# Kernel tuning notes

Hardware: AMD Instinct MI355X
Metric: run time of the kernel (lower is better)

The kernel has to match this reference:

```python
import math
import jax, jax.numpy as jnp
import numpy as np

H = 16
D_MODEL = 1024
D_K = D_MODEL // H


def setup_inputs() -> dict:
    key = jax.random.key(0)
    ks = jax.random.split(key, 12)
    B, S = 4, 2048
    scale = 1.0 / math.sqrt(D_MODEL)
    inp = {
        "query": jax.random.normal(ks[0], (B, S, D_MODEL), jnp.float32),
        "key": jax.random.normal(ks[1], (B, S, D_MODEL), jnp.float32),
        "value": jax.random.normal(ks[2], (B, S, D_MODEL), jnp.float32),
        "mask": jnp.ones((B, 1, 1, S), jnp.int32),
        "Wq": jax.random.normal(ks[3], (D_MODEL, D_MODEL), jnp.float32) * scale,
        "bq": jnp.zeros((D_MODEL,), jnp.float32),
        "Wk": jax.random.normal(ks[4], (D_MODEL, D_MODEL), jnp.float32) * scale,
        "bk": jnp.zeros((D_MODEL,), jnp.float32),
        "Wv": jax.random.normal(ks[5], (D_MODEL, D_MODEL), jnp.float32) * scale,
        "bv": jnp.zeros((D_MODEL,), jnp.float32),
        "Wo": jax.random.normal(ks[6], (D_MODEL, D_MODEL), jnp.float32) * scale,
        "bo": jnp.zeros((D_MODEL,), jnp.float32),
    }
    return inp


def _split_heads(x, W, b):
    # x: (B, S, d_model) -> (B, H, S, d_k); torch Linear: x @ W.T + b
    B, S, _ = x.shape
    y = x @ W.T + b
    return y.reshape(B, S, H, D_K).transpose(0, 2, 1, 3)


def reference(query, key, value, mask, Wq, bq, Wk, bk, Wv, bv, Wo, bo):
    B, Sq, _ = query.shape
    q = _split_heads(query, Wq, bq)   # (B,H,Sq,dk)
    k = _split_heads(key, Wk, bk)     # (B,H,Skv,dk)
    v = _split_heads(value, Wv, bv)   # (B,H,Skv,dk)
    scores = jnp.einsum('bhqd,bhkd->bhqk', q, k) / math.sqrt(D_K)
    scores = jnp.where(mask == 0, jnp.float32(-1e9), scores)
    p_attn = jax.nn.softmax(scores, axis=-1)  # dropout p=0 (eval)
    x = jnp.einsum('bhqk,bhkd->bhqd', p_attn, v)
    x = x.transpose(0, 2, 1, 3).reshape(B, Sq, H * D_K)
    return x @ Wo.T + bo
```

## Files before the change

### kernel.cpp

```cpp
#include <hip/hip_runtime.h>
#include <hip/hip_bf16.h>
#include <stdint.h>

typedef unsigned short u16;
typedef short bf16x8 __attribute__((ext_vector_type(8)));
typedef float f32x4 __attribute__((ext_vector_type(4)));

#define D_MODEL 1024
#define NHEAD 16
#define DK 64
#define SEQ 2048
#define NB 4
#define MTOT (NB * SEQ)

__device__ __forceinline__ u16 f2bf(float f) {
  union { float f; unsigned u; } x; x.f = f;
  unsigned r = x.u + 0x7FFFu + ((x.u >> 16) & 1u);
  return (u16)(r >> 16);
}
#if __has_builtin(__builtin_amdgcn_cvt_pk_bf16_f32)
__device__ __forceinline__ unsigned pkbf(float a, float b) {
  auto r = __builtin_amdgcn_cvt_pk_bf16_f32(a, b);
  union { decltype(r) v; unsigned u; } c; c.v = r; return c.u;
}
#else
__device__ __forceinline__ unsigned pkbf(float a, float b) {
  return (unsigned)f2bf(a) | ((unsigned)f2bf(b) << 16);
}
#endif
#if __has_builtin(__builtin_amdgcn_exp2f)
__device__ __forceinline__ float exp2r(float x) { return __builtin_amdgcn_exp2f(x); }
#else
__device__ __forceinline__ float exp2r(float x) { return exp2f(x); }
#endif
__device__ __forceinline__ void gl_lds16(const u16* g, u16* s) {
  __builtin_amdgcn_global_load_lds(
      (const __attribute__((address_space(1))) void*)g,
      (__attribute__((address_space(3))) void*)s, 16, 0, 0);
}

struct CvtArgs {
  const float4* s[7];
  uint2* d[7];
  int n4[7];
};
__global__ __launch_bounds__(256) void cvt_all(CvtArgs a) {
  const int y = blockIdx.y;
  const float4* s = a.s[y];
  uint2* d = a.d[y];
  const int n4 = a.n4[y];
  for (int i = blockIdx.x * 256 + threadIdx.x; i < n4; i += gridDim.x * 256) {
    float4 x = s[i];
    uint2 o;
    o.x = pkbf(x.x, x.y);
    o.y = pkbf(x.z, x.w);
    d[i] = o;
  }
}

template <int MODE>
__device__ __forceinline__ void gemm_body(
    const u16* __restrict__ A, const u16* __restrict__ W,
    const float* __restrict__ bias, void* __restrict__ out, float scale,
    int m0, int n0, u16* smem)
{
  u16* As = smem;
  u16* Bs = smem + 8192;

  const int tid = threadIdx.x;
  const int l = tid & 63, w = tid >> 6;
  const int wm = (w >> 1) << 6, wn = (w & 1) << 6;

  int srow[4], sk8[4], sdst[4];
#pragma unroll
  for (int r = 0; r < 4; ++r) {
    int c = r * 256 + tid;
    srow[r] = c >> 3;
    sk8[r] = (c & 7) ^ (srow[r] & 7);
    sdst[r] = c << 3;
  }
  int aoff[4][2], boff[4][2];
#pragma unroll
  for (int i = 0; i < 4; ++i) {
    int mr = wm + (i << 4) + (l & 15);
    int nr = wn + (i << 4) + (l & 15);
#pragma unroll
    for (int s = 0; s < 2; ++s) {
      int kc = (s << 2) + (l >> 4);
      aoff[i][s] = (mr << 6) + ((kc ^ (mr & 7)) << 3);
      boff[i][s] = (nr << 6) + ((kc ^ (nr & 7)) << 3);
    }
  }

  const u16* Ab = A + (size_t)m0 * D_MODEL;
  const u16* Bb = W + (size_t)n0 * D_MODEL;

  f32x4 acc[4][4] = {};

  for (int kt = 0; kt < 16; ++kt) {
    const int kbase = kt << 6;
#pragma unroll
    for (int r = 0; r < 4; ++r)
      gl_lds16(Ab + (size_t)srow[r] * D_MODEL + kbase + (sk8[r] << 3), As + sdst[r]);
#pragma unroll
    for (int r = 0; r < 4; ++r)
      gl_lds16(Bb + (size_t)srow[r] * D_MODEL + kbase + (sk8[r] << 3), Bs + sdst[r]);
    __syncthreads();
#pragma unroll
    for (int s = 0; s < 2; ++s) {
      bf16x8 af[4], bfv[4];
#pragma unroll
      for (int i = 0; i < 4; ++i) af[i] = *(const bf16x8*)(As + aoff[i][s]);
#pragma unroll
      for (int j = 0; j < 4; ++j) bfv[j] = *(const bf16x8*)(Bs + boff[j][s]);
#pragma unroll
      for (int i = 0; i < 4; ++i)
#pragma unroll
        for (int j = 0; j < 4; ++j)
          acc[i][j] = __builtin_amdgcn_mfma_f32_16x16x32_bf16(af[i], bfv[j], acc[i][j], 0, 0, 0);
    }
    __syncthreads();
  }

  if (MODE == 1) {
    u16* Cs = smem;
    u16* outb = (u16*)out;
#pragma unroll
    for (int i = 0; i < 4; ++i)
#pragma unroll
      for (int j = 0; j < 4; ++j) {
        int sl = wm + (i << 4) + ((l >> 4) << 2);
        int nl = wn + (j << 4) + (l & 15);
        float bj = bias[n0 + nl];
        uint2 pk;
        pk.x = pkbf(acc[i][j][0] + bj, acc[i][j][1] + bj);
        pk.y = pkbf(acc[i][j][2] + bj, acc[i][j][3] + bj);
        *(uint2*)(Cs + nl * 136 + sl) = pk;
      }
    __syncthreads();
    int nl = tid >> 1, sh = (tid & 1) << 6;
    int n = n0 + nl;
    int b_ = m0 >> 11;
    const uint4* src = (const uint4*)(Cs + nl * 136 + sh);
    uint4* dst = (uint4*)(outb +
        (((size_t)b_ * NHEAD + (n >> 6)) * DK + (n & 63)) * SEQ + (m0 & 2047) + sh);
#pragma unroll
    for (int e = 0; e < 8; ++e) dst[e] = src[e];
  } else {
    u16* outb = (u16*)out;
    float* outf = (float*)out;
#pragma unroll
    for (int i = 0; i < 4; ++i)
#pragma unroll
      for (int j = 0; j < 4; ++j) {
        int ml = m0 + wm + (i << 4) + ((l >> 4) << 2);
        int n = n0 + wn + (j << 4) + (l & 15);
        float bj = bias[n];
#pragma unroll
        for (int r = 0; r < 4; ++r) {
          int m = ml + r;
          float v = (acc[i][j][r] + bj) * scale;
          if (MODE == 0)
            outb[(((size_t)(m >> 11) * NHEAD + (n >> 6)) * SEQ + (m & 2047)) * DK + (n & 63)] = f2bf(v);
          else
            outf[(size_t)m * D_MODEL + n] = v;
        }
      }
  }
}

template <int MODE>
__global__ __launch_bounds__(256) void gemm128(
    const u16* __restrict__ A, const u16* __restrict__ W,
    const float* __restrict__ bias, void* __restrict__ out, float scale)
{
  __shared__ alignas(16) u16 smem[17408];
  gemm_body<MODE>(A, W, bias, out, scale,
                  blockIdx.x << 7, blockIdx.y << 7, smem);
}

__global__ __launch_bounds__(256) void proj_qkv(
    const u16* __restrict__ Cq, const u16* __restrict__ Ck, const u16* __restrict__ Cv,
    const u16* __restrict__ wq, const u16* __restrict__ wk, const u16* __restrict__ wv,
    const float* __restrict__ bq, const float* __restrict__ bk, const float* __restrict__ bv,
    u16* __restrict__ Qb, u16* __restrict__ Kb, u16* __restrict__ Vt, float scq)
{
  __shared__ alignas(16) u16 smem[17408];
  const int z = blockIdx.z;
  const int m0 = blockIdx.x << 7, n0 = blockIdx.y << 7;
  if (z == 0)
    gemm_body<0>(Cq, wq, bq, Qb, scq, m0, n0, smem);
  else if (z == 1)
    gemm_body<0>(Ck, wk, bk, Kb, 1.0f, m0, n0, smem);
  else
    gemm_body<1>(Cv, wv, bv, Vt, 1.0f, m0, n0, smem);
}

__global__ __launch_bounds__(256, 4) void attn_fused(
    const u16* __restrict__ Q,
    const u16* __restrict__ K,
    const u16* __restrict__ Vt,
    const int* __restrict__ mask,
    u16* __restrict__ X)
{
  __shared__ alignas(16) u16 PQ[8192];
  __shared__ alignas(16) u16 Ks[4096];
  __shared__ alignas(16) u16 Vs[5120];
  __shared__ alignas(16) float mbf[64];

  const int tid = threadIdx.x;
  const int l = tid & 63, w = tid >> 6;
  const int lq = l & 15, qd = l >> 4;
  const int bh = blockIdx.x;
  const int q0 = blockIdx.y << 7;
  const int b_ = bh >> 4, h = bh & 15;
  const size_t base = (size_t)bh * SEQ * DK;
  const int wq0 = w << 5;

#pragma unroll
  for (int r = 0; r < 4; ++r) {
    int c = r * 256 + tid;
    int row = c >> 3, k8 = (c & 7) ^ (row & 7);
    gl_lds16(Q + base + (size_t)(q0 + row) * DK + (k8 << 3), PQ + (c << 3));
  }
  {
    unsigned v = (tid < 16) ? 0x3F803F80u : 0u;
    uint2 pk; pk.x = v; pk.y = v;
    *(uint2*)(Vs + 4096 + tid * 4) = pk;
  }
  __syncthreads();

  bf16x8 qf[2][2];
#pragma unroll
  for (int i = 0; i < 2; ++i)
#pragma unroll
    for (int s = 0; s < 2; ++s) {
      int row = wq0 + (i << 4) + lq;
      qf[i][s] = *(const bf16x8*)(PQ + (row << 6) + ((((s << 2) + qd) ^ (row & 7)) << 3));
    }

  f32x4 Ov[2][4] = {};
  f32x4 Ovl[2] = {};

  for (int t = 0; t < 32; ++t) {
    const int kv0 = t << 6;
    __syncthreads();
#pragma unroll
    for (int r = 0; r < 2; ++r) {
      int c = r * 256 + tid;
      int row = c >> 3, k8 = (c & 7) ^ (row & 7);
      gl_lds16(K + base + (size_t)(kv0 + row) * DK + (k8 << 3), Ks + (c << 3));
    }
#pragma unroll
    for (int r = 0; r < 2; ++r) {
      int c = r * 256 + tid;
      int row = c >> 3, k8 = (c & 7) ^ (row & 7);
      gl_lds16(Vt + base + (size_t)row * SEQ + kv0 + (k8 << 3), Vs + (c << 3));
    }
    if (tid < 64)
      mbf[tid] = mask[b_ * SEQ + kv0 + tid] ? 0.0f : -1.44269504e9f;
    __syncthreads();

    float4 m4[4];
#pragma unroll
    for (int jb = 0; jb < 4; ++jb) m4[jb] = *(const float4*)(mbf + (jb << 4) + (qd << 2));

    f32x4 Sc[4][2];
#pragma unroll
    for (int jb = 0; jb < 4; ++jb)
#pragma unroll
      for (int i = 0; i < 2; ++i) {
        Sc[jb][i][0] = m4[jb].x; Sc[jb][i][1] = m4[jb].y;
        Sc[jb][i][2] = m4[jb].z; Sc[jb][i][3] = m4[jb].w;
      }
#pragma unroll
    for (int s = 0; s < 2; ++s) {
      bf16x8 kf[4];
#pragma unroll
      for (int jb = 0; jb < 4; ++jb) {
        int row = (jb << 4) + lq;
        kf[jb] = *(const bf16x8*)(Ks + (row << 6) + ((((s << 2) + qd) ^ (row & 7)) << 3));
      }
#pragma unroll
      for (int jb = 0; jb < 4; ++jb)
#pragma unroll
        for (int i = 0; i < 2; ++i)
          Sc[jb][i] = __builtin_amdgcn_mfma_f32_16x16x32_bf16(kf[jb], qf[i][s], Sc[jb][i], 0, 0, 0);
    }

#pragma unroll
    for (int i = 0; i < 2; ++i) {
      const int prow = wq0 + (i << 4) + lq;
      const int rbase = prow << 6;
      const int rsw = prow & 7;
#pragma unroll
      for (int jb = 0; jb < 4; ++jb) {
        float p0 = exp2r(Sc[jb][i][0]);
        float p1 = exp2r(Sc[jb][i][1]);
        float p2 = exp2r(Sc[jb][i][2]);
        float p3 = exp2r(Sc[jb][i][3]);
        uint2 pk;
        pk.x = pkbf(p0, p1);
        pk.y = pkbf(p2, p3);
        int c = (jb << 1) + (qd >> 1);
        *(uint2*)(PQ + rbase + ((c ^ rsw) << 3) + ((qd & 1) << 2)) = pk;
      }
    }

#pragma unroll
    for (int s = 0; s < 2; ++s) {
      bf16x8 pf[2], vf[4], vf1;
#pragma unroll
      for (int i = 0; i < 2; ++i) {
        int prow = wq0 + (i << 4) + lq;
        pf[i] = *(const bf16x8*)(PQ + (prow << 6) + ((((s << 2) + qd) ^ (prow & 7)) << 3));
      }
#pragma unroll
      for (int j = 0; j < 4; ++j) {
        int row = (j << 4) + lq;
        vf[j] = *(const bf16x8*)(Vs + (row << 6) + ((((s << 2) + qd) ^ (row & 7)) << 3));
      }
      {
        int row = 64 + lq;
        vf1 = *(const bf16x8*)(Vs + (row << 6) + ((((s << 2) + qd) ^ (row & 7)) << 3));
      }
#pragma unroll
      for (int i = 0; i < 2; ++i) {
#pragma unroll
        for (int j = 0; j < 4; ++j)
          Ov[i][j] = __builtin_amdgcn_mfma_f32_16x16x32_bf16(pf[i], vf[j], Ov[i][j], 0, 0, 0);
        Ovl[i] = __builtin_amdgcn_mfma_f32_16x16x32_bf16(pf[i], vf1, Ovl[i], 0, 0, 0);
      }
    }
  }

#pragma unroll
  for (int i = 0; i < 2; ++i) {
    float inv[4];
#pragma unroll
    for (int r = 0; r < 4; ++r) inv[r] = 1.0f / Ovl[i][r];
#pragma unroll
    for (int r = 0; r < 4; ++r) {
      float sc_ = __shfl(inv[r], l & 48);
      int qrow = q0 + wq0 + (i << 4) + (qd << 2) + r;
#pragma unroll
      for (int j = 0; j < 4; ++j)
        X[((size_t)b_ * SEQ + qrow) * D_MODEL + (h << 6) + (j << 4) + lq] =
            f2bf(Ov[i][j][r] * sc_);
    }
  }
}

extern "C" void kernel_launch(void* const* d_in, const int* in_sizes, int n_in,
                              void* d_out, int out_size, void* d_ws, size_t ws_size,
                              hipStream_t stream) {
  const float* query = (const float*)d_in[0];
  const float* key_  = (const float*)d_in[1];
  const float* value = (const float*)d_in[2];
  const int* mask    = (const int*)d_in[3];
  const float* Wq = (const float*)d_in[4];
  const float* bq = (const float*)d_in[5];
  const float* Wk = (const float*)d_in[6];
  const float* bk = (const float*)d_in[7];
  const float* Wv = (const float*)d_in[8];
  const float* bv = (const float*)d_in[9];
  const float* Wo = (const float*)d_in[10];
  const float* bo = (const float*)d_in[11];

  u16* ws16 = (u16*)d_ws;
  const size_t WSZ = (size_t)D_MODEL * D_MODEL;
  const size_t ASZ = (size_t)MTOT * D_MODEL;
  const float SCQ = 0.125f * 1.44269504088896f;

  dim3 blk(256);
  dim3 gg(MTOT / 128, D_MODEL / 128);

  if (ws_size >= (size_t)(4 * WSZ + 4 * ASZ) * 2) {
    u16* wqc = ws16;
    u16* wkc = ws16 + WSZ;
    u16* wvc = ws16 + 2 * WSZ;
    u16* woc = ws16 + 3 * WSZ;
    u16* Cq  = ws16 + 4 * WSZ;
    u16* Ck  = ws16 + 4 * WSZ + ASZ;
    u16* Qb  = ws16 + 4 * WSZ + 2 * ASZ;
    u16* Kb  = ws16 + 4 * WSZ + 3 * ASZ;
    u16* Xb  = Cq;
    u16* Vtb = (u16*)d_out;
    u16* Cv  = (u16*)d_out + ASZ;

    CvtArgs ca;
    ca.s[0] = (const float4*)query; ca.d[0] = (uint2*)Cq;  ca.n4[0] = (int)(ASZ / 4);
    ca.s[1] = (const float4*)key_;  ca.d[1] = (uint2*)Ck;  ca.n4[1] = (int)(ASZ / 4);
    ca.s[2] = (const float4*)value; ca.d[2] = (uint2*)Cv;  ca.n4[2] = (int)(ASZ / 4);
    ca.s[3] = (const float4*)Wq;    ca.d[3] = (uint2*)wqc; ca.n4[3] = (int)(WSZ / 4);
    ca.s[4] = (const float4*)Wk;    ca.d[4] = (uint2*)wkc; ca.n4[4] = (int)(WSZ / 4);
    ca.s[5] = (const float4*)Wv;    ca.d[5] = (uint2*)wvc; ca.n4[5] = (int)(WSZ / 4);
    ca.s[6] = (const float4*)Wo;    ca.d[6] = (uint2*)woc; ca.n4[6] = (int)(WSZ / 4);

    cvt_all<<<dim3(512, 7), blk, 0, stream>>>(ca);
    proj_qkv<<<dim3(MTOT / 128, D_MODEL / 128, 3), blk, 0, stream>>>(
        Cq, Ck, Cv, wqc, wkc, wvc, bq, bk, bv, Qb, Kb, Vtb, SCQ);
    attn_fused<<<dim3(NB * NHEAD, SEQ / 128), blk, 0, stream>>>(Qb, Kb, Vtb, mask, Xb);
    gemm128<2><<<gg, blk, 0, stream>>>(Xb, woc, bo, d_out, 1.0f);
  } else {
    u16* wqc = ws16;
    u16* wkc = ws16 + WSZ;
    u16* wvc = ws16 + 2 * WSZ;
    u16* woc = ws16 + 3 * WSZ;
    u16* C1  = ws16 + 4 * WSZ;
    u16* Qb  = ws16 + 4 * WSZ + ASZ;
    u16* Kb  = ws16 + 4 * WSZ + 2 * ASZ;
    u16* Xb  = C1;
    u16* Vtb = (u16*)d_out;

    CvtArgs cw;
    for (int i = 0; i < 7; ++i) { cw.s[i] = (const float4*)Wq; cw.d[i] = (uint2*)wqc; cw.n4[i] = 0; }
    cw.s[0] = (const float4*)Wq; cw.d[0] = (uint2*)wqc; cw.n4[0] = (int)(WSZ / 4);
    cw.s[1] = (const float4*)Wk; cw.d[1] = (uint2*)wkc; cw.n4[1] = (int)(WSZ / 4);
    cw.s[2] = (const float4*)Wv; cw.d[2] = (uint2*)wvc; cw.n4[2] = (int)(WSZ / 4);
    cw.s[3] = (const float4*)Wo; cw.d[3] = (uint2*)woc; cw.n4[3] = (int)(WSZ / 4);

    cvt_all<<<dim3(512, 4), blk, 0, stream>>>(cw);
    CvtArgs c1;
    c1.s[0] = (const float4*)query; c1.d[0] = (uint2*)C1; c1.n4[0] = (int)(ASZ / 4);
    cvt_all<<<dim3(1024, 1), blk, 0, stream>>>(c1);
    gemm128<0><<<gg, blk, 0, stream>>>(C1, wqc, bq, Qb, SCQ);
    c1.s[0] = (const float4*)key_;
    cvt_all<<<dim3(1024, 1), blk, 0, stream>>>(c1);
    gemm128<0><<<gg, blk, 0, stream>>>(C1, wkc, bk, Kb, 1.0f);
    c1.s[0] = (const float4*)value;
    cvt_all<<<dim3(1024, 1), blk, 0, stream>>>(c1);
    gemm128<1><<<gg, blk, 0, stream>>>(C1, wvc, bv, Vtb, 1.0f);
    attn_fused<<<dim3(NB * NHEAD, SEQ / 128), blk, 0, stream>>>(Qb, Kb, Vtb, mask, Xb);
    gemm128<2><<<gg, blk, 0, stream>>>(Xb, woc, bo, d_out, 1.0f);
  }
}
```

Baseline: 342.9 us.

## Double-buffer K/V tiles and widen attention blocks to 256 query rows

The attention kernel now runs 512-thread blocks that each cover 256 query rows, so every K/V tile loaded into shared memory is reused by eight waves instead of four. K, V and the mask tile are double-buffered: the next tile is fetched while the current one is computed, leaving one barrier per iteration instead of two. The all-ones row used to accumulate softmax denominators moves to its own small buffer. In exchange, shared memory per block grows to roughly 66 KB and the grid has half as many blocks, which reduces resident blocks per CU and the parallelism available for hiding latency.

```diff
diff --git a/kernel.cpp b/kernel.cpp
--- a/kernel.cpp
+++ b/kernel.cpp
@@ -196,38 +196,45 @@
     gemm_body<1>(Cv, wv, bv, Vt, 1.0f, m0, n0, smem);
 }
 
-__global__ __launch_bounds__(256, 4) void attn_fused(
+__global__ __launch_bounds__(512, 4) void attn_fused(
     const u16* __restrict__ Q,
     const u16* __restrict__ K,
     const u16* __restrict__ Vt,
     const int* __restrict__ mask,
     u16* __restrict__ X)
 {
-  __shared__ alignas(16) u16 PQ[8192];
-  __shared__ alignas(16) u16 Ks[4096];
-  __shared__ alignas(16) u16 Vs[5120];
-  __shared__ alignas(16) float mbf[64];
+  __shared__ alignas(16) u16 PQ[16384];
+  __shared__ alignas(16) u16 Ks[2][4096];
+  __shared__ alignas(16) u16 Vs[2][4096];
+  __shared__ alignas(16) u16 On[1024];
+  __shared__ alignas(16) float mbf[2][64];
 
   const int tid = threadIdx.x;
   const int l = tid & 63, w = tid >> 6;
   const int lq = l & 15, qd = l >> 4;
   const int bh = blockIdx.x;
-  const int q0 = blockIdx.y << 7;
+  const int q0 = blockIdx.y << 8;
   const int b_ = bh >> 4, h = bh & 15;
   const size_t base = (size_t)bh * SEQ * DK;
   const int wq0 = w << 5;
 
 #pragma unroll
   for (int r = 0; r < 4; ++r) {
-    int c = r * 256 + tid;
+    int c = r * 512 + tid;
     int row = c >> 3, k8 = (c & 7) ^ (row & 7);
     gl_lds16(Q + base + (size_t)(q0 + row) * DK + (k8 << 3), PQ + (c << 3));
   }
-  {
+  if (tid < 256) {
     unsigned v = (tid < 16) ? 0x3F803F80u : 0u;
     uint2 pk; pk.x = v; pk.y = v;
-    *(uint2*)(Vs + 4096 + tid * 4) = pk;
-  }
+    *(uint2*)(On + tid * 4) = pk;
+  }
+  {
+    int row = tid >> 3, k8 = (tid & 7) ^ (row & 7);
+    gl_lds16(K + base + (size_t)row * DK + (k8 << 3), Ks[0] + (tid << 3));
+    gl_lds16(Vt + base + (size_t)row * SEQ + (k8 << 3), Vs[0] + (tid << 3));
+  }
+  if (tid < 64) mbf[0][tid] = mask[b_ * SEQ + tid] ? 0.0f : -1.44269504e9f;
   __syncthreads();
 
   bf16x8 qf[2][2];
@@ -243,27 +250,18 @@
   f32x4 Ovl[2] = {};
 
   for (int t = 0; t < 32; ++t) {
-    const int kv0 = t << 6;
-    __syncthreads();
-#pragma unroll
-    for (int r = 0; r < 2; ++r) {
-      int c = r * 256 + tid;
-      int row = c >> 3, k8 = (c & 7) ^ (row & 7);
-      gl_lds16(K + base + (size_t)(kv0 + row) * DK + (k8 << 3), Ks + (c << 3));
-    }
-#pragma unroll
-    for (int r = 0; r < 2; ++r) {
-      int c = r * 256 + tid;
-      int row = c >> 3, k8 = (c & 7) ^ (row & 7);
-      gl_lds16(Vt + base + (size_t)row * SEQ + kv0 + (k8 << 3), Vs + (c << 3));
-    }
-    if (tid < 64)
-      mbf[tid] = mask[b_ * SEQ + kv0 + tid] ? 0.0f : -1.44269504e9f;
-    __syncthreads();
+    const int cur = t & 1;
+    if (t + 1 < 32) {
+      const int kv1 = (t + 1) << 6;
+      int row = tid >> 3, k8 = (tid & 7) ^ (row & 7);
+      gl_lds16(K + base + (size_t)(kv1 + row) * DK + (k8 << 3), Ks[cur ^ 1] + (tid << 3));
+      gl_lds16(Vt + base + (size_t)row * SEQ + kv1 + (k8 << 3), Vs[cur ^ 1] + (tid << 3));
+      if (tid < 64) mbf[cur ^ 1][tid] = mask[b_ * SEQ + kv1 + tid] ? 0.0f : -1.44269504e9f;
+    }
 
     float4 m4[4];
 #pragma unroll
-    for (int jb = 0; jb < 4; ++jb) m4[jb] = *(const float4*)(mbf + (jb << 4) + (qd << 2));
+    for (int jb = 0; jb < 4; ++jb) m4[jb] = *(const float4*)(mbf[cur] + (jb << 4) + (qd << 2));
 
     f32x4 Sc[4][2];
 #pragma unroll
@@ -273,13 +271,15 @@
         Sc[jb][i][0] = m4[jb].x; Sc[jb][i][1] = m4[jb].y;
         Sc[jb][i][2] = m4[jb].z; Sc[jb][i][3] = m4[jb].w;
       }
+    const u16* Kc = Ks[cur];
+    const u16* Vc = Vs[cur];
 #pragma unroll
     for (int s = 0; s < 2; ++s) {
       bf16x8 kf[4];
 #pragma unroll
       for (int jb = 0; jb < 4; ++jb) {
         int row = (jb << 4) + lq;
-        kf[jb] = *(const bf16x8*)(Ks + (row << 6) + ((((s << 2) + qd) ^ (row & 7)) << 3));
+        kf[jb] = *(const bf16x8*)(Kc + (row << 6) + ((((s << 2) + qd) ^ (row & 7)) << 3));
       }
 #pragma unroll
       for (int jb = 0; jb < 4; ++jb)
@@ -318,12 +318,9 @@
 #pragma unroll
       for (int j = 0; j < 4; ++j) {
         int row = (j << 4) + lq;
-        vf[j] = *(const bf16x8*)(Vs + (row << 6) + ((((s << 2) + qd) ^ (row & 7)) << 3));
-      }
-      {
-        int row = 64 + lq;
-        vf1 = *(const bf16x8*)(Vs + (row << 6) + ((((s << 2) + qd) ^ (row & 7)) << 3));
-      }
+        vf[j] = *(const bf16x8*)(Vc + (row << 6) + ((((s << 2) + qd) ^ (row & 7)) << 3));
+      }
+      vf1 = *(const bf16x8*)(On + (lq << 6) + ((((s << 2) + qd) ^ (lq & 7)) << 3));
 #pragma unroll
       for (int i = 0; i < 2; ++i) {
 #pragma unroll
@@ -332,6 +329,7 @@
         Ovl[i] = __builtin_amdgcn_mfma_f32_16x16x32_bf16(pf[i], vf1, Ovl[i], 0, 0, 0);
       }
     }
+    __syncthreads();
   }
 
 #pragma unroll
@@ -400,7 +398,7 @@
     cvt_all<<<dim3(512, 7), blk, 0, stream>>>(ca);
     proj_qkv<<<dim3(MTOT / 128, D_MODEL / 128, 3), blk, 0, stream>>>(
         Cq, Ck, Cv, wqc, wkc, wvc, bq, bk, bv, Qb, Kb, Vtb, SCQ);
-    attn_fused<<<dim3(NB * NHEAD, SEQ / 128), blk, 0, stream>>>(Qb, Kb, Vtb, mask, Xb);
+    attn_fused<<<dim3(NB * NHEAD, SEQ / 256), dim3(512), 0, stream>>>(Qb, Kb, Vtb, mask, Xb);
     gemm128<2><<<gg, blk, 0, stream>>>(Xb, woc, bo, d_out, 1.0f);
   } else {
     u16* wqc = ws16;
@@ -431,7 +429,7 @@
     c1.s[0] = (const float4*)value;
     cvt_all<<<dim3(1024, 1), blk, 0, stream>>>(c1);
     gemm128<1><<<gg, blk, 0, stream>>>(C1, wvc, bv, Vtb, 1.0f);
-    attn_fused<<<dim3(NB * NHEAD, SEQ / 128), blk, 0, stream>>>(Qb, Kb, Vtb, mask, Xb);
+    attn_fused<<<dim3(NB * NHEAD, SEQ / 256), dim3(512), 0, stream>>>(Qb, Kb, Vtb, mask, Xb);
     gemm128<2><<<gg, blk, 0, stream>>>(Xb, woc, bo, d_out, 1.0f);
   }
 }
```

Result: faster. 335.8 us (-2.1%).
